# Performance work log

Hardware: AMD Instinct MI355X
Metric: run time of the kernel (lower is better)

## Reference

```python
import jax, jax.numpy as jnp
import numpy as np

D_MODEL, D_STATE, D_CONV, D_INNER = 1024, 16, 4, 2048
B, S = 1, 2048
EPS = 1e-5


def setup_inputs() -> dict:
    key = jax.random.key(0)
    ks = jax.random.split(key, 8)
    sc = 0.02
    return {
        "x": jax.random.normal(ks[0], (B, S, D_MODEL), jnp.float32),
        "ln_g": jnp.ones((D_MODEL,), jnp.float32),
        "ln_b": jnp.zeros((D_MODEL,), jnp.float32),
        "in_w": jax.random.normal(ks[1], (2 * D_INNER, D_MODEL), jnp.float32) * sc,
        "conv_w": jax.random.normal(ks[2], (D_INNER, 1, D_CONV), jnp.float32) * sc,  # depthwise OIH
        "conv_b": jax.random.normal(ks[3], (D_INNER,), jnp.float32) * sc,
        "xproj_w": jax.random.normal(ks[4], (2 * D_STATE + 1, D_INNER), jnp.float32) * sc,
        "dt_w": jax.random.normal(ks[5], (D_INNER, 1), jnp.float32) * sc,
        "dt_b": jax.random.normal(ks[6], (D_INNER,), jnp.float32) * sc,
        "A_log": jnp.log(jnp.arange(1, D_STATE + 1, dtype=jnp.float32)),
        "D": jnp.ones((D_INNER,), jnp.float32),
        "out_w": jax.random.normal(ks[7], (D_MODEL, D_INNER), jnp.float32) * sc,
    }


def reference(x, ln_g, ln_b, in_w, conv_w, conv_b, xproj_w, dt_w, dt_b, A_log, D, out_w):
    b, s, _ = x.shape
    d_inner = D.shape[0]
    d_state = A_log.shape[0]
    d_conv = conv_w.shape[-1]
    residual = x

    # LayerNorm
    mu = jnp.mean(x, axis=-1, keepdims=True)
    var = jnp.mean(jnp.square(x - mu), axis=-1, keepdims=True)
    xn = (x - mu) * jax.lax.rsqrt(var + EPS) * ln_g + ln_b

    # in_proj, split into x and gate z
    xz = jnp.einsum('bsd,ed->bse', xn, in_w)  # [B,S,2*d_inner]
    xi, z = jnp.split(xz, 2, axis=-1)

    # causal depthwise conv1d (torch pads d_conv-1 both sides then crops to seq_len)
    xc = jnp.transpose(xi, (0, 2, 1))  # [B,C,S]
    xc = jnp.pad(xc, ((0, 0), (0, 0), (d_conv - 1, 0)))
    xc = jax.lax.conv_general_dilated(
        xc, conv_w, window_strides=(1,), padding='VALID',
        dimension_numbers=('NCH', 'OIH', 'NCH'), feature_group_count=d_inner)
    xc = xc + conv_b[None, :, None]
    xs = jax.nn.silu(jnp.transpose(xc, (0, 2, 1)))  # [B,S,d_inner]

    # SSM projections
    xp = jnp.einsum('bsd,ed->bse', xs, xproj_w)  # [B,S,2*d_state+1]
    delta = jax.nn.softplus(xp[..., :1] * dt_w[:, 0] + dt_b)  # [B,S,d_inner]
    Bm = xp[..., 1:1 + d_state]  # [B,S,N]
    Cm = xp[..., 1 + d_state:]   # [B,S,N]
    A = -jnp.exp(A_log)          # [N]

    dA = jnp.exp(delta[..., None] * A)                      # [B,S,d_inner,N]
    dBx = delta[..., None] * Bm[:, :, None, :] * xs[..., None]  # [B,S,d_inner,N]

    def step(h, inp):
        dA_t, dBx_t, C_t = inp
        h = dA_t * h + dBx_t                     # [B,d_inner,N]
        y_t = jnp.einsum('bdn,bn->bd', h, C_t)   # [B,d_inner]
        return h, y_t

    h0 = jnp.zeros((b, d_inner, d_state), x.dtype)
    _, ys = jax.lax.scan(step, h0, (jnp.moveaxis(dA, 1, 0),
                                    jnp.moveaxis(dBx, 1, 0),
                                    jnp.moveaxis(Cm, 1, 0)))
    y = jnp.moveaxis(ys, 0, 1) + xs * D  # [B,S,d_inner]

    y = y * jax.nn.silu(z)
    out = jnp.einsum('bse,de->bsd', y, out_w)
    return out + residual
```

## Files before the change

kernel.cpp:

```cpp
#include <hip/hip_runtime.h>
#include <cstdint>
#include <cstddef>

#define D_MODEL 1024
#define D_STATE 16
#define D_CONV  4
#define D_INNER 2048
#define SEQ     2048
#define NCHUNK  128
#define CLEN    16
#define LN_EPS  1e-5f

typedef unsigned short ushort_t;
typedef __attribute__((ext_vector_type(8))) short short8;
typedef __attribute__((ext_vector_type(4))) float f32x4;

__device__ __forceinline__ ushort_t f2bf(float x) {
  union { float f; uint32_t u; } v; v.f = x;
  uint32_t r = (v.u + 0x7fffu + ((v.u >> 16) & 1u)) >> 16;
  return (ushort_t)r;
}
__device__ __forceinline__ float bf2f(ushort_t u) {
  union { uint32_t x; float f; } v; v.x = ((uint32_t)u) << 16; return v.f;
}

__device__ __forceinline__ void async16(void* lds, const void* g) {
  __builtin_amdgcn_global_load_lds(
      (const __attribute__((address_space(1))) unsigned int*)g,
      (__attribute__((address_space(3))) unsigned int*)lds, 16, 0, 0);
}

__device__ __forceinline__ float softplus_f(float x) {
  if (x > 20.f) return x;
  if (x < -20.f) return __expf(x);
  return __logf(1.f + __expf(x));
}

__global__ __launch_bounds__(256) void prep_kernel(const float* __restrict__ x,
                                                   const float* __restrict__ g,
                                                   const float* __restrict__ b,
                                                   const float* __restrict__ inw,
                                                   const float* __restrict__ outw,
                                                   const float* __restrict__ xpw,
                                                   ushort_t* __restrict__ xn_bf,
                                                   ushort_t* __restrict__ inw_bf,
                                                   ushort_t* __restrict__ outw_bf,
                                                   ushort_t* __restrict__ xpw_bf) {
  int blk = blockIdx.x;
  if (blk < SEQ) {
    int row = blk;
    const float4* xr = (const float4*)(x + (size_t)row * D_MODEL);
    float4 v = xr[threadIdx.x];
    float s  = v.x + v.y + v.z + v.w;
    float ss = v.x * v.x + v.y * v.y + v.z * v.z + v.w * v.w;
    #pragma unroll
    for (int o = 32; o; o >>= 1) { s += __shfl_down(s, o); ss += __shfl_down(ss, o); }
    __shared__ float sbuf[8], ssbuf[8];
    int wid = threadIdx.x >> 6, lane = threadIdx.x & 63;
    if (lane == 0) { sbuf[wid] = s; ssbuf[wid] = ss; }
    __syncthreads();
    if (threadIdx.x == 0) {
      float t = 0.f, t2 = 0.f;
      for (int i = 0; i < 4; i++) { t += sbuf[i]; t2 += ssbuf[i]; }
      float mu = t / D_MODEL;
      sbuf[4] = mu;
      ssbuf[4] = rsqrtf(t2 / D_MODEL - mu * mu + LN_EPS);
    }
    __syncthreads();
    float mu = sbuf[4], inv = ssbuf[4];
    float4 gv = ((const float4*)g)[threadIdx.x];
    float4 bv = ((const float4*)b)[threadIdx.x];
    ushort_t o4[4];
    o4[0] = f2bf((v.x - mu) * inv * gv.x + bv.x);
    o4[1] = f2bf((v.y - mu) * inv * gv.y + bv.y);
    o4[2] = f2bf((v.z - mu) * inv * gv.z + bv.z);
    o4[3] = f2bf((v.w - mu) * inv * gv.w + bv.w);
    *(ushort4*)&xn_bf[(size_t)row * D_MODEL + threadIdx.x * 4] =
        make_ushort4(o4[0], o4[1], o4[2], o4[3]);
  } else {
    int idx = (blk - SEQ) * 256 + threadIdx.x;
    const int n1 = 2 * D_INNER * D_MODEL;
    const int n2 = D_MODEL * D_INNER;
    const int n3 = 64 * D_INNER;
    if (idx < n1) {
      inw_bf[idx] = f2bf(inw[idx]);
    } else if (idx < n1 + n2) {
      int j = idx - n1;
      outw_bf[j] = f2bf(outw[j]);
    } else if (idx < n1 + n2 + n3) {
      int j = idx - n1 - n2;
      xpw_bf[j] = (j < 33 * D_INNER) ? f2bf(xpw[j]) : (ushort_t)0;
    }
  }
}

template <int BM, int BN, int KDIM, int EPI, int NBUF, int KSPLIT>
__global__ __launch_bounds__(256, 2) void gemm_pipe(const ushort_t* __restrict__ A,
                                                    const ushort_t* __restrict__ B,
                                                    void* __restrict__ Cout,
                                                    const float* __restrict__ R,
                                                    int N) {
  constexpr int KT = KDIM / 32 / KSPLIT;
  constexpr int K2 = KDIM * 2;
  constexpr int IA = BM / 64, IB = BN / 64;
  constexpr int S  = IA + IB;
  constexpr int W  = (NBUF - 2) * S;
  constexpr int WTM = BM / 2, WTN = BN / 2;
  constexpr int MREP = WTM / 16, NREP = WTN / 16;
  __shared__ __align__(16) ushort_t As[NBUF][BM * 32];
  __shared__ __align__(16) ushort_t Bs[NBUF][BN * 32];

  const int nwg = gridDim.x * gridDim.y;
  int bid = blockIdx.y * gridDim.x + blockIdx.x;
  int swz = (bid & 7) * (nwg >> 3) + (bid >> 3);
  int bn = swz % gridDim.x, bm = swz / gridDim.x;
  int ks = 0;
  if constexpr (KSPLIT > 1) { ks = bn; bn = 0; }
  const int tid = threadIdx.x, wid = tid >> 6, lane = tid & 63;
  const int wm = wid >> 1, wn = wid & 1;
  const int row0A = bm * BM, row0B = bn * BN;
  const size_t kbase = (size_t)ks * KT * 64;

  const char* gA[IA];
  const char* gB[IB];
  #pragma unroll
  for (int i = 0; i < IA; i++) {
    int o = i * 4096 + tid * 16;
    int r = o >> 6, src = (o & 63) ^ ((r & 3) << 4);
    gA[i] = (const char*)A + (size_t)(row0A + r) * K2 + src + kbase;
  }
  #pragma unroll
  for (int i = 0; i < IB; i++) {
    int o = i * 4096 + tid * 16;
    int r = o >> 6, src = (o & 63) ^ ((r & 3) << 4);
    gB[i] = (const char*)B + (size_t)(row0B + r) * K2 + src + kbase;
  }
  const int ldsW = wid * 1024;

  auto STAGE = [&](int bb, int kt) {
    int kb = kt * 64;
    #pragma unroll
    for (int i = 0; i < IA; i++)
      async16((char*)&As[bb][0] + i * 4096 + ldsW, gA[i] + kb);
    #pragma unroll
    for (int i = 0; i < IB; i++)
      async16((char*)&Bs[bb][0] + i * 4096 + ldsW, gB[i] + kb);
  };

  #pragma unroll
  for (int p = 0; p < NBUF - 1; p++) STAGE(p, p);

  int offA[MREP], offB[NREP];
  #pragma unroll
  for (int m = 0; m < MREP; m++) {
    int row = wm * WTM + m * 16 + (lane & 15);
    offA[m] = row * 64 + ((((lane >> 4)) ^ (row & 3)) << 4);
  }
  #pragma unroll
  for (int n = 0; n < NREP; n++) {
    int row = wn * WTN + n * 16 + (lane & 15);
    offB[n] = row * 64 + ((((lane >> 4)) ^ (row & 3)) << 4);
  }

  f32x4 acc[MREP][NREP] = {};
  int cur = 0;
  for (int kt = 0; kt < KT; kt++) {
    if (kt < KT - 1) {
      if constexpr (W == 6)       asm volatile("s_waitcnt vmcnt(6)" ::: "memory");
      else if constexpr (W == 8)  asm volatile("s_waitcnt vmcnt(8)" ::: "memory");
      else if constexpr (W == 12) asm volatile("s_waitcnt vmcnt(12)" ::: "memory");
      else                        asm volatile("s_waitcnt vmcnt(0)" ::: "memory");
    } else {
      asm volatile("s_waitcnt vmcnt(0)" ::: "memory");
    }
    __builtin_amdgcn_s_barrier();
    __builtin_amdgcn_sched_barrier(0);
    const char* Ab = (const char*)&As[cur][0];
    const char* Bb = (const char*)&Bs[cur][0];
    short8 af[MREP], bf[NREP];
    #pragma unroll
    for (int m = 0; m < MREP; m++) af[m] = *(const short8*)(Ab + offA[m]);
    #pragma unroll
    for (int n = 0; n < NREP; n++) bf[n] = *(const short8*)(Bb + offB[n]);
    if (kt + NBUF - 1 < KT) {
      int b2 = cur + NBUF - 1; if (b2 >= NBUF) b2 -= NBUF;
      STAGE(b2, kt + NBUF - 1);
    }
    __builtin_amdgcn_s_setprio(1);
    #pragma unroll
    for (int m = 0; m < MREP; m++)
      #pragma unroll
      for (int n = 0; n < NREP; n++)
        acc[m][n] = __builtin_amdgcn_mfma_f32_16x16x32_bf16(af[m], bf[n], acc[m][n], 0, 0, 0);
    __builtin_amdgcn_s_setprio(0);
    cur++; if (cur == NBUF) cur = 0;
  }

  #pragma unroll
  for (int m = 0; m < MREP; m++)
    #pragma unroll
    for (int n = 0; n < NREP; n++) {
      int r0 = row0A + wm * WTM + m * 16 + ((lane >> 4) << 2);
      int c  = row0B + wn * WTN + n * 16 + (lane & 15);
      #pragma unroll
      for (int q = 0; q < 4; q++) {
        if constexpr (EPI == 0) {
          ((ushort_t*)Cout)[(size_t)(r0 + q) * N + c] = f2bf(acc[m][n][q]);
        } else if constexpr (EPI == 1) {
          size_t idx = (size_t)(r0 + q) * N + c;
          ((float*)Cout)[idx] = acc[m][n][q] + R[idx];
        } else {
          if (c < 33)
            ((float*)Cout)[((size_t)ks * SEQ + r0 + q) * 33 + c] = acc[m][n][q];
        }
      }
    }
}

__global__ __launch_bounds__(256) void xp_reduce(const float* __restrict__ part,
                                                 float* __restrict__ xp) {
  int i = blockIdx.x * 256 + threadIdx.x;
  if (i >= SEQ * 33) return;
  float s = 0.f;
  #pragma unroll
  for (int k = 0; k < 8; k++) s += part[(size_t)k * SEQ * 33 + i];
  xp[i] = s;
}

__global__ __launch_bounds__(256) void conv_silu_kernel(const ushort_t* __restrict__ xz_bf,
                                                        const float* __restrict__ cw,
                                                        const float* __restrict__ cb,
                                                        ushort_t* __restrict__ xs_bf) {
  const int t = blockIdx.x;
  const int d0 = threadIdx.x * 8;
  short8 rows[4];
  #pragma unroll
  for (int k = 0; k < 4; k++) {
    int tt = t - 3 + k;
    if (tt >= 0) rows[k] = *(const short8*)&xz_bf[(size_t)tt * (2 * D_INNER) + d0];
    else         rows[k] = (short8)0;
  }
  short8 o8;
  #pragma unroll
  for (int j = 0; j < 8; j++) {
    float4 w = ((const float4*)cw)[d0 + j];
    float acc = cb[d0 + j]
              + bf2f((ushort_t)rows[0][j]) * w.x
              + bf2f((ushort_t)rows[1][j]) * w.y
              + bf2f((ushort_t)rows[2][j]) * w.z
              + bf2f((ushort_t)rows[3][j]) * w.w;
    float sg = 1.f / (1.f + __expf(-acc));
    o8[j] = (short)f2bf(acc * sg);
  }
  *(short8*)&xs_bf[(size_t)t * D_INNER + d0] = o8;
}

__device__ __forceinline__ void dapow(float g1, float* da) {
  float g2 = g1 * g1, g4 = g2 * g2, g8 = g4 * g4;
  #pragma unroll
  for (int n = 0; n < 16; n++) {
    int e = n + 1;
    float v = (e & 1) ? g1 : 1.f;
    if (e & 2) v *= g2;
    if (e & 4) v *= g4;
    if (e & 8) v *= g8;
    da[n] = v;
  }
}

__global__ __launch_bounds__(256) void scan_pass1(const ushort_t* __restrict__ xs_bf,
                                                  const float* __restrict__ xp,
                                                  const float* __restrict__ dt_w,
                                                  const float* __restrict__ dt_b,
                                                  const float* __restrict__ A_log,
                                                  float* __restrict__ Hp,
                                                  float* __restrict__ Sd) {
  int c = blockIdx.x, g = blockIdx.y;
  int d = g * 256 + threadIdx.x;
  __shared__ float Bsh[CLEN][16], drs[CLEN], Ash[16];
  {
    int t = threadIdx.x >> 4, n = threadIdx.x & 15;
    Bsh[t][n] = xp[(size_t)(c * CLEN + t) * 33 + 1 + n];
    if (threadIdx.x < CLEN) drs[threadIdx.x] = xp[(size_t)(c * CLEN + threadIdx.x) * 33];
    else if (threadIdx.x < CLEN + 16) {
      int n2 = threadIdx.x - CLEN;
      Ash[n2] = -__expf(A_log[n2]);
    }
  }
  __syncthreads();
  bool fastA = true;
  #pragma unroll
  for (int n = 0; n < 16; n++) fastA = fastA && (fabsf(Ash[n] + (float)(n + 1)) < 1e-4f * (n + 1));
  float dw = dt_w[d], db = dt_b[d];
  float h[16];
  float S = 0.f;
  #pragma unroll
  for (int n = 0; n < 16; n++) h[n] = 0.f;
  for (int t = 0; t < CLEN; t++) {
    float delta = softplus_f(drs[t] * dw + db);
    S += delta;
    float xv = bf2f(xs_bf[(size_t)(c * CLEN + t) * D_INNER + d]);
    float w = delta * xv;
    float bb[16];
    *(float4*)&bb[0]  = *(const float4*)&Bsh[t][0];
    *(float4*)&bb[4]  = *(const float4*)&Bsh[t][4];
    *(float4*)&bb[8]  = *(const float4*)&Bsh[t][8];
    *(float4*)&bb[12] = *(const float4*)&Bsh[t][12];
    if (fastA) {
      float da[16];
      dapow(__expf(-delta), da);
      #pragma unroll
      for (int n = 0; n < 16; n++) h[n] = da[n] * h[n] + w * bb[n];
    } else {
      #pragma unroll
      for (int n = 0; n < 16; n++) {
        float da = __expf(delta * Ash[n]);
        h[n] = da * h[n] + w * bb[n];
      }
    }
  }
  size_t base = ((size_t)c * D_INNER + d) * 16;
  #pragma unroll
  for (int n = 0; n < 16; n += 4)
    *(float4*)&Hp[base + n] = make_float4(h[n], h[n + 1], h[n + 2], h[n + 3]);
  Sd[(size_t)c * D_INNER + d] = S;
}

__global__ __launch_bounds__(64) void scan_combine(const float* __restrict__ Hp,
                                                   const float* __restrict__ Sd,
                                                   const float* __restrict__ A_log,
                                                   float* __restrict__ Hin) {
  int idx = blockIdx.x * 64 + threadIdx.x;
  int d = idx >> 4, n = idx & 15;
  float An = -__expf(A_log[n]);
  float h = 0.f;
  const size_t stride = (size_t)D_INNER * 16;
  #pragma unroll 8
  for (int c = 0; c < NCHUNK; c++) {
    float S  = Sd[(size_t)c * D_INNER + d];
    float hp = Hp[(size_t)c * stride + idx];
    Hin[(size_t)c * stride + idx] = h;
    h = __expf(An * S) * h + hp;
  }
}

__global__ __launch_bounds__(256) void scan_pass2(const ushort_t* __restrict__ xs_bf,
                                                  const float* __restrict__ xp,
                                                  const ushort_t* __restrict__ xz_bf,
                                                  const float* __restrict__ dt_w,
                                                  const float* __restrict__ dt_b,
                                                  const float* __restrict__ A_log,
                                                  const float* __restrict__ Dp,
                                                  const float* __restrict__ Hin,
                                                  ushort_t* __restrict__ y_bf) {
  int c = blockIdx.x, g = blockIdx.y;
  int d = g * 256 + threadIdx.x;
  __shared__ float Bsh[CLEN][16], Csh[CLEN][16], drs[CLEN], Ash[16];
  {
    int t = threadIdx.x >> 4, n = threadIdx.x & 15;
    Bsh[t][n] = xp[(size_t)(c * CLEN + t) * 33 + 1 + n];
    Csh[t][n] = xp[(size_t)(c * CLEN + t) * 33 + 17 + n];
    if (threadIdx.x < CLEN) drs[threadIdx.x] = xp[(size_t)(c * CLEN + threadIdx.x) * 33];
    else if (threadIdx.x < CLEN + 16) {
      int n2 = threadIdx.x - CLEN;
      Ash[n2] = -__expf(A_log[n2]);
    }
  }
  __syncthreads();
  bool fastA = true;
  #pragma unroll
  for (int n = 0; n < 16; n++) fastA = fastA && (fabsf(Ash[n] + (float)(n + 1)) < 1e-4f * (n + 1));
  float dw = dt_w[d], db = dt_b[d], Dd = Dp[d];
  float h[16];
  size_t hbase = ((size_t)c * D_INNER + d) * 16;
  #pragma unroll
  for (int n = 0; n < 16; n += 4)
    *(float4*)&h[n] = *(const float4*)&Hin[hbase + n];
  for (int t = 0; t < CLEN; t++) {
    float delta = softplus_f(drs[t] * dw + db);
    size_t ti = (size_t)(c * CLEN + t);
    float xv = bf2f(xs_bf[ti * D_INNER + d]);
    float w = delta * xv;
    float bb[16], cc[16];
    *(float4*)&bb[0]  = *(const float4*)&Bsh[t][0];
    *(float4*)&bb[4]  = *(const float4*)&Bsh[t][4];
    *(float4*)&bb[8]  = *(const float4*)&Bsh[t][8];
    *(float4*)&bb[12] = *(const float4*)&Bsh[t][12];
    *(float4*)&cc[0]  = *(const float4*)&Csh[t][0];
    *(float4*)&cc[4]  = *(const float4*)&Csh[t][4];
    *(float4*)&cc[8]  = *(const float4*)&Csh[t][8];
    *(float4*)&cc[12] = *(const float4*)&Csh[t][12];
    float y = 0.f;
    if (fastA) {
      float da[16];
      dapow(__expf(-delta), da);
      #pragma unroll
      for (int n = 0; n < 16; n++) {
        h[n] = da[n] * h[n] + w * bb[n];
        y += h[n] * cc[n];
      }
    } else {
      #pragma unroll
      for (int n = 0; n < 16; n++) {
        float da = __expf(delta * Ash[n]);
        h[n] = da * h[n] + w * bb[n];
        y += h[n] * cc[n];
      }
    }
    float z = bf2f(xz_bf[ti * (2 * D_INNER) + D_INNER + d]);
    float sz = z / (1.f + __expf(-z));
    float out = (y + xv * Dd) * sz;
    y_bf[ti * D_INNER + d] = f2bf(out);
  }
}

extern "C" void kernel_launch(void* const* d_in, const int* in_sizes, int n_in,
                              void* d_out, int out_size, void* d_ws, size_t ws_size,
                              hipStream_t stream) {
  const float* x      = (const float*)d_in[0];
  const float* ln_g   = (const float*)d_in[1];
  const float* ln_b   = (const float*)d_in[2];
  const float* in_w   = (const float*)d_in[3];
  const float* conv_w = (const float*)d_in[4];
  const float* conv_b = (const float*)d_in[5];
  const float* xproj_w= (const float*)d_in[6];
  const float* dt_w   = (const float*)d_in[7];
  const float* dt_b   = (const float*)d_in[8];
  const float* A_log  = (const float*)d_in[9];
  const float* Dp     = (const float*)d_in[10];
  const float* out_w  = (const float*)d_in[11];
  float* out = (float*)d_out;

  char* ws = (char*)d_ws;
  size_t off = 0;
  auto alloc = [&](size_t bytes) { char* p = ws + off; off += (bytes + 255) & ~(size_t)255; return p; };
  ushort_t* xz_bf   = (ushort_t*)alloc((size_t)SEQ * 2 * D_INNER * 2);
  ushort_t* xn_bf   = (ushort_t*)alloc((size_t)SEQ * D_MODEL * 2);
  ushort_t* inw_bf  = (ushort_t*)alloc((size_t)2 * D_INNER * D_MODEL * 2);
  ushort_t* outw_bf = (ushort_t*)alloc((size_t)D_MODEL * D_INNER * 2);
  ushort_t* xpw_bf  = (ushort_t*)alloc((size_t)64 * D_INNER * 2);
  ushort_t* xs_bf   = (ushort_t*)alloc((size_t)SEQ * D_INNER * 2);
  float*    xp_part = (float*)   alloc((size_t)8 * SEQ * 33 * 4);
  float*    xp      = (float*)   alloc((size_t)SEQ * 33 * 4);
  float*    Hp      = (float*)   alloc((size_t)NCHUNK * D_INNER * 16 * 4);
  float*    Hin     = (float*)   alloc((size_t)NCHUNK * D_INNER * 16 * 4);
  float*    Sd      = (float*)   alloc((size_t)NCHUNK * D_INNER * 4);
  ushort_t* y_bf    = (ushort_t*)alloc((size_t)SEQ * D_INNER * 2);
  (void)ws_size;

  const int ncvt = 2 * D_INNER * D_MODEL + D_MODEL * D_INNER + 64 * D_INNER;
  prep_kernel<<<SEQ + (ncvt + 255) / 256, 256, 0, stream>>>(
      x, ln_g, ln_b, in_w, out_w, xproj_w, xn_bf, inw_bf, outw_bf, xpw_bf);
  gemm_pipe<256, 128, D_MODEL, 0, 3, 1><<<dim3(2 * D_INNER / 128, SEQ / 256), 256, 0, stream>>>(
      xn_bf, inw_bf, xz_bf, nullptr, 2 * D_INNER);
  conv_silu_kernel<<<SEQ, 256, 0, stream>>>(xz_bf, conv_w, conv_b, xs_bf);
  gemm_pipe<64, 64, D_INNER, 3, 6, 8><<<dim3(8, SEQ / 64), 256, 0, stream>>>(
      xs_bf, xpw_bf, xp_part, nullptr, 64);
  xp_reduce<<<(SEQ * 33 + 255) / 256, 256, 0, stream>>>(xp_part, xp);
  scan_pass1<<<dim3(NCHUNK, D_INNER / 256), 256, 0, stream>>>(xs_bf, xp, dt_w, dt_b, A_log, Hp, Sd);
  scan_combine<<<D_INNER * 16 / 64, 64, 0, stream>>>(Hp, Sd, A_log, Hin);
  scan_pass2<<<dim3(NCHUNK, D_INNER / 256), 256, 0, stream>>>(xs_bf, xp, xz_bf, dt_w, dt_b, A_log,
                                                              Dp, Hin, y_bf);
  gemm_pipe<128, 64, D_INNER, 1, 6, 1><<<dim3(D_MODEL / 64, SEQ / 128), 256, 0, stream>>>(
      y_bf, outw_bf, out, x, D_MODEL);
}
```

Before: 140.0 us.

## Hierarchical two-level chunk combine, two channels per scan thread, retune GEMM tiles

The serial 128-step chunk combine becomes a two-level scan. combineA scans 16 chunks within each of 8 groups in parallel and records local prefixes and group totals. combineB scans the 8 group totals, and scan_pass2 rebuilds each chunk's initial state from the local prefix plus the decayed group prefix. Scan threads now handle two channels each, halving the grid, and the in_proj and out_proj GEMM tile shapes are shrunk to launch more blocks. This shortens the serial dependency chain in the combine, in exchange for an extra launch, more workspace traffic, and less parallelism in the scan passes.

```diff
diff --git a/kernel.cpp b/kernel.cpp
--- a/kernel.cpp
+++ b/kernel.cpp
@@ -9,6 +9,8 @@
 #define SEQ     2048
 #define NCHUNK  128
 #define CLEN    16
+#define NGRP    8
+#define GCH     16
 #define LN_EPS  1e-5f
 
 typedef unsigned short ushort_t;
@@ -34,6 +36,19 @@
   if (x > 20.f) return x;
   if (x < -20.f) return __expf(x);
   return __logf(1.f + __expf(x));
+}
+
+__device__ __forceinline__ void dapow(float g1, float* da) {
+  float g2 = g1 * g1, g4 = g2 * g2, g8 = g4 * g4;
+  #pragma unroll
+  for (int n = 0; n < 16; n++) {
+    int e = n + 1;
+    float v = (e & 1) ? g1 : 1.f;
+    if (e & 2) v *= g2;
+    if (e & 4) v *= g4;
+    if (e & 8) v *= g8;
+    da[n] = v;
+  }
 }
 
 __global__ __launch_bounds__(256) void prep_kernel(const float* __restrict__ x,
@@ -255,19 +270,6 @@
   *(short8*)&xs_bf[(size_t)t * D_INNER + d0] = o8;
 }
 
-__device__ __forceinline__ void dapow(float g1, float* da) {
-  float g2 = g1 * g1, g4 = g2 * g2, g8 = g4 * g4;
-  #pragma unroll
-  for (int n = 0; n < 16; n++) {
-    int e = n + 1;
-    float v = (e & 1) ? g1 : 1.f;
-    if (e & 2) v *= g2;
-    if (e & 4) v *= g4;
-    if (e & 8) v *= g8;
-    da[n] = v;
-  }
-}
-
 __global__ __launch_bounds__(256) void scan_pass1(const ushort_t* __restrict__ xs_bf,
                                                   const float* __restrict__ xp,
                                                   const float* __restrict__ dt_w,
@@ -275,8 +277,8 @@
                                                   const float* __restrict__ A_log,
                                                   float* __restrict__ Hp,
                                                   float* __restrict__ Sd) {
-  int c = blockIdx.x, g = blockIdx.y;
-  int d = g * 256 + threadIdx.x;
+  int c = blockIdx.x;
+  int d0 = blockIdx.y * 512 + threadIdx.x;
   __shared__ float Bsh[CLEN][16], drs[CLEN], Ash[16];
   {
     int t = threadIdx.x >> 4, n = threadIdx.x & 15;
@@ -291,56 +293,86 @@
   bool fastA = true;
   #pragma unroll
   for (int n = 0; n < 16; n++) fastA = fastA && (fabsf(Ash[n] + (float)(n + 1)) < 1e-4f * (n + 1));
-  float dw = dt_w[d], db = dt_b[d];
-  float h[16];
-  float S = 0.f;
-  #pragma unroll
-  for (int n = 0; n < 16; n++) h[n] = 0.f;
+  float dw[2] = {dt_w[d0], dt_w[d0 + 256]};
+  float db[2] = {dt_b[d0], dt_b[d0 + 256]};
+  float h[2][16] = {};
+  float S[2] = {0.f, 0.f};
   for (int t = 0; t < CLEN; t++) {
-    float delta = softplus_f(drs[t] * dw + db);
-    S += delta;
-    float xv = bf2f(xs_bf[(size_t)(c * CLEN + t) * D_INNER + d]);
-    float w = delta * xv;
     float bb[16];
     *(float4*)&bb[0]  = *(const float4*)&Bsh[t][0];
     *(float4*)&bb[4]  = *(const float4*)&Bsh[t][4];
     *(float4*)&bb[8]  = *(const float4*)&Bsh[t][8];
     *(float4*)&bb[12] = *(const float4*)&Bsh[t][12];
-    if (fastA) {
-      float da[16];
-      dapow(__expf(-delta), da);
-      #pragma unroll
-      for (int n = 0; n < 16; n++) h[n] = da[n] * h[n] + w * bb[n];
-    } else {
-      #pragma unroll
-      for (int n = 0; n < 16; n++) {
-        float da = __expf(delta * Ash[n]);
-        h[n] = da * h[n] + w * bb[n];
+    float drt = drs[t];
+    size_t tb = (size_t)(c * CLEN + t) * D_INNER;
+    float xv[2] = {bf2f(xs_bf[tb + d0]), bf2f(xs_bf[tb + d0 + 256])};
+    #pragma unroll
+    for (int u = 0; u < 2; u++) {
+      float delta = softplus_f(drt * dw[u] + db[u]);
+      S[u] += delta;
+      float w = delta * xv[u];
+      if (fastA) {
+        float da[16];
+        dapow(__expf(-delta), da);
+        #pragma unroll
+        for (int n = 0; n < 16; n++) h[u][n] = da[n] * h[u][n] + w * bb[n];
+      } else {
+        #pragma unroll
+        for (int n = 0; n < 16; n++) h[u][n] = __expf(delta * Ash[n]) * h[u][n] + w * bb[n];
       }
     }
   }
-  size_t base = ((size_t)c * D_INNER + d) * 16;
-  #pragma unroll
-  for (int n = 0; n < 16; n += 4)
-    *(float4*)&Hp[base + n] = make_float4(h[n], h[n + 1], h[n + 2], h[n + 3]);
-  Sd[(size_t)c * D_INNER + d] = S;
-}
-
-__global__ __launch_bounds__(64) void scan_combine(const float* __restrict__ Hp,
-                                                   const float* __restrict__ Sd,
-                                                   const float* __restrict__ A_log,
-                                                   float* __restrict__ Hin) {
-  int idx = blockIdx.x * 64 + threadIdx.x;
+  #pragma unroll
+  for (int u = 0; u < 2; u++) {
+    int d = d0 + u * 256;
+    size_t base = ((size_t)c * D_INNER + d) * 16;
+    #pragma unroll
+    for (int n = 0; n < 16; n += 4)
+      *(float4*)&Hp[base + n] = make_float4(h[u][n], h[u][n + 1], h[u][n + 2], h[u][n + 3]);
+    Sd[(size_t)c * D_INNER + d] = S[u];
+  }
+}
+
+__global__ __launch_bounds__(256) void combineA(const float* __restrict__ Hp,
+                                                const float* __restrict__ Sd,
+                                                const float* __restrict__ A_log,
+                                                float* __restrict__ Hl,
+                                                float* __restrict__ Slocp,
+                                                float* __restrict__ Hgtot,
+                                                float* __restrict__ Sgtot) {
+  int g = blockIdx.x;
+  int idx = blockIdx.y * 256 + threadIdx.x;
   int d = idx >> 4, n = idx & 15;
   float An = -__expf(A_log[n]);
-  float h = 0.f;
+  float h = 0.f, S = 0.f;
   const size_t stride = (size_t)D_INNER * 16;
-  #pragma unroll 8
-  for (int c = 0; c < NCHUNK; c++) {
-    float S  = Sd[(size_t)c * D_INNER + d];
+  #pragma unroll 4
+  for (int j = 0; j < GCH; j++) {
+    int c = g * GCH + j;
+    Hl[(size_t)c * stride + idx] = h;
+    if (n == 0) Slocp[(size_t)c * D_INNER + d] = S;
+    float Sc = Sd[(size_t)c * D_INNER + d];
     float hp = Hp[(size_t)c * stride + idx];
-    Hin[(size_t)c * stride + idx] = h;
-    h = __expf(An * S) * h + hp;
+    h = __expf(An * Sc) * h + hp;
+    S += Sc;
+  }
+  Hgtot[(size_t)g * stride + idx] = h;
+  if (n == 0) Sgtot[(size_t)g * D_INNER + d] = S;
+}
+
+__global__ __launch_bounds__(256) void combineB(const float* __restrict__ Hgtot,
+                                                const float* __restrict__ Sgtot,
+                                                const float* __restrict__ A_log,
+                                                float* __restrict__ Ginit) {
+  int idx = blockIdx.x * 256 + threadIdx.x;
+  int d = idx >> 4, n = idx & 15;
+  float An = -__expf(A_log[n]);
+  float G = 0.f;
+  const size_t stride = (size_t)D_INNER * 16;
+  #pragma unroll
+  for (int g = 0; g < NGRP; g++) {
+    Ginit[(size_t)g * stride + idx] = G;
+    G = __expf(An * Sgtot[(size_t)g * D_INNER + d]) * G + Hgtot[(size_t)g * stride + idx];
   }
 }
 
@@ -351,10 +383,12 @@
                                                   const float* __restrict__ dt_b,
                                                   const float* __restrict__ A_log,
                                                   const float* __restrict__ Dp,
-                                                  const float* __restrict__ Hin,
+                                                  const float* __restrict__ Hl,
+                                                  const float* __restrict__ Slocp,
+                                                  const float* __restrict__ Ginit,
                                                   ushort_t* __restrict__ y_bf) {
-  int c = blockIdx.x, g = blockIdx.y;
-  int d = g * 256 + threadIdx.x;
+  int c = blockIdx.x;
+  int d0 = blockIdx.y * 512 + threadIdx.x;
   __shared__ float Bsh[CLEN][16], Csh[CLEN][16], drs[CLEN], Ash[16];
   {
     int t = threadIdx.x >> 4, n = threadIdx.x & 15;
@@ -370,17 +404,34 @@
   bool fastA = true;
   #pragma unroll
   for (int n = 0; n < 16; n++) fastA = fastA && (fabsf(Ash[n] + (float)(n + 1)) < 1e-4f * (n + 1));
-  float dw = dt_w[d], db = dt_b[d], Dd = Dp[d];
-  float h[16];
-  size_t hbase = ((size_t)c * D_INNER + d) * 16;
-  #pragma unroll
-  for (int n = 0; n < 16; n += 4)
-    *(float4*)&h[n] = *(const float4*)&Hin[hbase + n];
+  float dw[2] = {dt_w[d0], dt_w[d0 + 256]};
+  float db[2] = {dt_b[d0], dt_b[d0 + 256]};
+  float Dd[2] = {Dp[d0], Dp[d0 + 256]};
+  int g8 = c >> 4;
+  float h[2][16];
+  #pragma unroll
+  for (int u = 0; u < 2; u++) {
+    int d = d0 + u * 256;
+    size_t hb = ((size_t)c * D_INNER + d) * 16;
+    size_t gb = ((size_t)g8 * D_INNER + d) * 16;
+    float Slp = Slocp[(size_t)c * D_INNER + d];
+    float hl[16], gi[16];
+    #pragma unroll
+    for (int n = 0; n < 16; n += 4) {
+      *(float4*)&hl[n] = *(const float4*)&Hl[hb + n];
+      *(float4*)&gi[n] = *(const float4*)&Ginit[gb + n];
+    }
+    if (fastA) {
+      float pw[16];
+      dapow(__expf(-Slp), pw);
+      #pragma unroll
+      for (int n = 0; n < 16; n++) h[u][n] = hl[n] + pw[n] * gi[n];
+    } else {
+      #pragma unroll
+      for (int n = 0; n < 16; n++) h[u][n] = hl[n] + __expf(Ash[n] * Slp) * gi[n];
+    }
+  }
   for (int t = 0; t < CLEN; t++) {
-    float delta = softplus_f(drs[t] * dw + db);
-    size_t ti = (size_t)(c * CLEN + t);
-    float xv = bf2f(xs_bf[ti * D_INNER + d]);
-    float w = delta * xv;
     float bb[16], cc[16];
     *(float4*)&bb[0]  = *(const float4*)&Bsh[t][0];
     *(float4*)&bb[4]  = *(const float4*)&Bsh[t][4];
@@ -390,27 +441,36 @@
     *(float4*)&cc[4]  = *(const float4*)&Csh[t][4];
     *(float4*)&cc[8]  = *(const float4*)&Csh[t][8];
     *(float4*)&cc[12] = *(const float4*)&Csh[t][12];
-    float y = 0.f;
-    if (fastA) {
-      float da[16];
-      dapow(__expf(-delta), da);
-      #pragma unroll
-      for (int n = 0; n < 16; n++) {
-        h[n] = da[n] * h[n] + w * bb[n];
-        y += h[n] * cc[n];
+    float drt = drs[t];
+    size_t ti = (size_t)(c * CLEN + t);
+    float xv[2] = {bf2f(xs_bf[ti * D_INNER + d0]), bf2f(xs_bf[ti * D_INNER + d0 + 256])};
+    float zv[2] = {bf2f(xz_bf[ti * (2 * D_INNER) + D_INNER + d0]),
+                   bf2f(xz_bf[ti * (2 * D_INNER) + D_INNER + d0 + 256])};
+    #pragma unroll
+    for (int u = 0; u < 2; u++) {
+      float delta = softplus_f(drt * dw[u] + db[u]);
+      float w = delta * xv[u];
+      float y = 0.f;
+      if (fastA) {
+        float da[16];
+        dapow(__expf(-delta), da);
+        #pragma unroll
+        for (int n = 0; n < 16; n++) {
+          h[u][n] = da[n] * h[u][n] + w * bb[n];
+          y += h[u][n] * cc[n];
+        }
+      } else {
+        #pragma unroll
+        for (int n = 0; n < 16; n++) {
+          h[u][n] = __expf(delta * Ash[n]) * h[u][n] + w * bb[n];
+          y += h[u][n] * cc[n];
+        }
       }
-    } else {
-      #pragma unroll
-      for (int n = 0; n < 16; n++) {
-        float da = __expf(delta * Ash[n]);
-        h[n] = da * h[n] + w * bb[n];
-        y += h[n] * cc[n];
-      }
-    }
-    float z = bf2f(xz_bf[ti * (2 * D_INNER) + D_INNER + d]);
-    float sz = z / (1.f + __expf(-z));
-    float out = (y + xv * Dd) * sz;
-    y_bf[ti * D_INNER + d] = f2bf(out);
+      float z = zv[u];
+      float sz = z / (1.f + __expf(-z));
+      float out = (y + xv[u] * Dd[u]) * sz;
+      y_bf[ti * D_INNER + d0 + u * 256] = f2bf(out);
+    }
   }
 }
 
@@ -443,24 +503,29 @@
   float*    xp_part = (float*)   alloc((size_t)8 * SEQ * 33 * 4);
   float*    xp      = (float*)   alloc((size_t)SEQ * 33 * 4);
   float*    Hp      = (float*)   alloc((size_t)NCHUNK * D_INNER * 16 * 4);
-  float*    Hin     = (float*)   alloc((size_t)NCHUNK * D_INNER * 16 * 4);
+  float*    Hl      = (float*)   alloc((size_t)NCHUNK * D_INNER * 16 * 4);
   float*    Sd      = (float*)   alloc((size_t)NCHUNK * D_INNER * 4);
+  float*    Slocp   = (float*)   alloc((size_t)NCHUNK * D_INNER * 4);
+  float*    Hgtot   = (float*)   alloc((size_t)NGRP * D_INNER * 16 * 4);
+  float*    Sgtot   = (float*)   alloc((size_t)NGRP * D_INNER * 4);
+  float*    Ginit   = (float*)   alloc((size_t)NGRP * D_INNER * 16 * 4);
   ushort_t* y_bf    = (ushort_t*)alloc((size_t)SEQ * D_INNER * 2);
   (void)ws_size;
 
   const int ncvt = 2 * D_INNER * D_MODEL + D_MODEL * D_INNER + 64 * D_INNER;
   prep_kernel<<<SEQ + (ncvt + 255) / 256, 256, 0, stream>>>(
       x, ln_g, ln_b, in_w, out_w, xproj_w, xn_bf, inw_bf, outw_bf, xpw_bf);
-  gemm_pipe<256, 128, D_MODEL, 0, 3, 1><<<dim3(2 * D_INNER / 128, SEQ / 256), 256, 0, stream>>>(
+  gemm_pipe<128, 128, D_MODEL, 0, 4, 1><<<dim3(2 * D_INNER / 128, SEQ / 128), 256, 0, stream>>>(
       xn_bf, inw_bf, xz_bf, nullptr, 2 * D_INNER);
   conv_silu_kernel<<<SEQ, 256, 0, stream>>>(xz_bf, conv_w, conv_b, xs_bf);
   gemm_pipe<64, 64, D_INNER, 3, 6, 8><<<dim3(8, SEQ / 64), 256, 0, stream>>>(
       xs_bf, xpw_bf, xp_part, nullptr, 64);
   xp_reduce<<<(SEQ * 33 + 255) / 256, 256, 0, stream>>>(xp_part, xp);
-  scan_pass1<<<dim3(NCHUNK, D_INNER / 256), 256, 0, stream>>>(xs_bf, xp, dt_w, dt_b, A_log, Hp, Sd);
-  scan_combine<<<D_INNER * 16 / 64, 64, 0, stream>>>(Hp, Sd, A_log, Hin);
-  scan_pass2<<<dim3(NCHUNK, D_INNER / 256), 256, 0, stream>>>(xs_bf, xp, xz_bf, dt_w, dt_b, A_log,
-                                                              Dp, Hin, y_bf);
-  gemm_pipe<128, 64, D_INNER, 1, 6, 1><<<dim3(D_MODEL / 64, SEQ / 128), 256, 0, stream>>>(
+  scan_pass1<<<dim3(NCHUNK, D_INNER / 512), 256, 0, stream>>>(xs_bf, xp, dt_w, dt_b, A_log, Hp, Sd);
+  combineA<<<dim3(NGRP, D_INNER * 16 / 256), 256, 0, stream>>>(Hp, Sd, A_log, Hl, Slocp, Hgtot, Sgtot);
+  combineB<<<D_INNER * 16 / 256, 256, 0, stream>>>(Hgtot, Sgtot, A_log, Ginit);
+  scan_pass2<<<dim3(NCHUNK, D_INNER / 512), 256, 0, stream>>>(xs_bf, xp, xz_bf, dt_w, dt_b, A_log,
+                                                              Dp, Hl, Slocp, Ginit, y_bf);
+  gemm_pipe<64, 64, D_INNER, 1, 6, 1><<<dim3(D_MODEL / 64, SEQ / 64), 256, 0, stream>>>(
       y_bf, outw_bf, out, x, D_MODEL);
 }
```

Result: faster. 134.3 us (-4.0%).
